# Kernel optimization log

Hardware: AMD Instinct MI355X
Metric: run time of the kernel (lower is better)

Reference implementation:

```python
import jax, jax.numpy as jnp
import numpy as np

NUM_EMB = 16384
EMB_DIM = 64
BETA = 0.25  # commitment_cost, legacy=True formulation


def _l2norm(x, axis=-1):
    # matches F.normalize(p=2): x / max(||x||, 1e-12)
    n = jnp.sqrt(jnp.sum(x * x, axis=axis, keepdims=True))
    return x / jnp.maximum(n, 1e-12)


def setup_inputs() -> dict:
    key = jax.random.key(0)
    k_z, k_cb, k_w, k_b = jax.random.split(key, 4)
    z = jax.random.normal(k_z, (16, 1024, EMB_DIM), dtype=jnp.float32)
    # frozen codebook: N(0, d^{-0.5})
    codebook = jax.random.normal(k_cb, (NUM_EMB, EMB_DIM), dtype=jnp.float32) * (EMB_DIM ** -0.5)
    # Linear(d, d) default init: U(-1/sqrt(d), 1/sqrt(d))
    lim = 1.0 / np.sqrt(EMB_DIM)
    proj_w = jax.random.uniform(k_w, (EMB_DIM, EMB_DIM), dtype=jnp.float32, minval=-lim, maxval=lim)
    proj_b = jax.random.uniform(k_b, (EMB_DIM,), dtype=jnp.float32, minval=-lim, maxval=lim)
    scale = jnp.float32(10.0)  # l2_norm_scale
    return {"z": z, "codebook": codebook, "proj_w": proj_w, "proj_b": proj_b, "scale": scale}


def reference(z, codebook, proj_w, proj_b, scale):
    B, T, d = z.shape
    zf = z.reshape(-1, d)                                   # [BT, d]
    quant_codebook = codebook @ proj_w.T + proj_b           # [N, d]
    zn = _l2norm(zf)
    cn = _l2norm(quant_codebook)
    distances = -jnp.einsum('bd,nd->bn', zn, cn) * scale    # [BT, N]
    idx = jnp.argmin(distances, axis=1)                     # [BT]
    quantized = quant_codebook[idx].reshape(z.shape)        # [B, T, d]
    sg = jax.lax.stop_gradient
    commitment_loss = jnp.mean((sg(quantized) - z) ** 2)
    codebook_loss = jnp.mean((quantized - sg(z)) ** 2)
    vq_loss = commitment_loss + BETA * codebook_loss        # legacy=True
    quantized_st = z + sg(quantized - z)                    # straight-through
    return quantized_st, vq_loss, idx.reshape(B, T)
```

## Files before the change

kernel.cpp:

```cpp
#include <hip/hip_runtime.h>
#include <hip/hip_bf16.h>


#define NCODES 16384
#define NTOK   16384
#define DIM    64
#define MARGIN_MFMA 8e-3f
#define CAP    16

typedef __attribute__((ext_vector_type(8))) short bf16x8;
typedef __attribute__((ext_vector_type(4))) float f32x4;
#define GLOBAL_AS __attribute__((address_space(1)))
#define LDS_AS    __attribute__((address_space(3)))

__device__ float  g_qcb[NCODES * DIM];
__device__ short  g_cnb[NCODES * DIM];
__device__ short  g_znb[NTOK * DIM];
__device__ unsigned g_topu[NTOK];
__device__ int    g_candcnt[NTOK];
__device__ int    g_cand[NTOK * CAP];
__device__ float  g_loss;
__device__ int    g_done;

__device__ __forceinline__ float wave_sum64(float v) {
#pragma unroll
  for (int o = 32; o > 0; o >>= 1) v += __shfl_xor(v, o, 64);
  return v;
}
__device__ __forceinline__ short f2bf(float f) {
  __hip_bfloat16 h = __float2bfloat16(f);
  return *reinterpret_cast<short*>(&h);
}
__device__ __forceinline__ float bf2f(short s) {
  __hip_bfloat16 h = *reinterpret_cast<__hip_bfloat16*>(&s);
  return __bfloat162float(h);
}
__device__ __forceinline__ void split8(const float* v, bf16x8& hi, bf16x8& lo) {
#pragma unroll
  for (int i = 0; i < 8; ++i) {
    float f = v[i];
    short h = f2bf(f);
    hi[i] = h;
    lo[i] = f2bf(f - bf2f(h));
  }
}

__global__ __launch_bounds__(256) void k_prep(const float* __restrict__ cb,
                                              const float* __restrict__ pw,
                                              const float* __restrict__ pb,
                                              const float* __restrict__ z) {
  int tid = threadIdx.x;
  int wave = tid >> 6, lane = tid & 63, quad = lane >> 4, col = lane & 15;
  if (blockIdx.x < 256) {
    int rowBase = blockIdx.x * 64 + wave * 16;
    const float* cr = cb + (size_t)(rowBase + col) * 64 + quad * 8;
    bf16x8 ah0, al0, ah1, al1;
    split8(cr, ah0, al0);
    split8(cr + 32, ah1, al1);
    float vals[4][4];
    float nr[4] = {0.f, 0.f, 0.f, 0.f};
    const f32x4 fz = {0.f, 0.f, 0.f, 0.f};
#pragma unroll
    for (int nt = 0; nt < 4; ++nt) {
      int j = col + 16 * nt;
      const float* wr = pw + (size_t)j * 64 + quad * 8;
      bf16x8 bh0, bl0, bh1, bl1;
      split8(wr, bh0, bl0);
      split8(wr + 32, bh1, bl1);
      f32x4 d = __builtin_amdgcn_mfma_f32_16x16x32_bf16(ah0, bh0, fz, 0, 0, 0);
      d = __builtin_amdgcn_mfma_f32_16x16x32_bf16(ah1, bh1, d, 0, 0, 0);
      d = __builtin_amdgcn_mfma_f32_16x16x32_bf16(ah0, bl0, d, 0, 0, 0);
      d = __builtin_amdgcn_mfma_f32_16x16x32_bf16(ah1, bl1, d, 0, 0, 0);
      d = __builtin_amdgcn_mfma_f32_16x16x32_bf16(al0, bh0, d, 0, 0, 0);
      d = __builtin_amdgcn_mfma_f32_16x16x32_bf16(al1, bh1, d, 0, 0, 0);
      float bj = pb[j];
#pragma unroll
      for (int r = 0; r < 4; ++r) {
        float v = d[r] + bj;
        vals[nt][r] = v;
        nr[r] = fmaf(v, v, nr[r]);
      }
    }
#pragma unroll
    for (int r = 0; r < 4; ++r) {
      float v = nr[r];
      v += __shfl_xor(v, 1, 64);
      v += __shfl_xor(v, 2, 64);
      v += __shfl_xor(v, 4, 64);
      v += __shfl_xor(v, 8, 64);
      nr[r] = 1.0f / fmaxf(sqrtf(v), 1e-12f);
    }
#pragma unroll
    for (int nt = 0; nt < 4; ++nt)
#pragma unroll
      for (int r = 0; r < 4; ++r) {
        int row = rowBase + quad * 4 + r;
        int j = col + 16 * nt;
        g_qcb[(size_t)row * 64 + j] = vals[nt][r];
        g_cnb[(size_t)row * 64 + j] = f2bf(vals[nt][r] * nr[r]);
      }
  } else {
    int zb = blockIdx.x - 256;
    int gid = zb * 256 + tid;
    if (gid < NTOK) { g_topu[gid] = 0u; g_candcnt[gid] = 0; }
    if (gid == 0) { g_loss = 0.f; g_done = 0; }
    int base = zb * 64;
    for (int r = 0; r < 16; ++r) {
      int row = base + wave * 16 + r;
      float v = z[(size_t)row * 64 + lane];
      float tot = wave_sum64(v * v);
      g_znb[(size_t)row * 64 + lane] = f2bf(v / fmaxf(sqrtf(tot), 1e-12f));
    }
  }
}

__global__ __launch_bounds__(256) void k_mfma1() {
  __shared__ __align__(16) short smB[2][8192];
  int tid = threadIdx.x;
  int wave = tid >> 6, lane = tid & 63;
  int quad = lane >> 4, col = lane & 15;
  int tokBlock = blockIdx.x >> 3, split = blockIdx.x & 7;
  int tokBase = tokBlock * 128 + wave * 32;

  const short* za = g_znb + (size_t)(tokBase + col) * 64 + quad * 8;
  bf16x8 A0[2], A1[2];
#pragma unroll
  for (int f = 0; f < 2; ++f) {
    A0[f] = *(const bf16x8*)(za + f * 16 * 64);
    A1[f] = *(const bf16x8*)(za + f * 16 * 64 + 32);
  }
  float m[2][4];
#pragma unroll
  for (int f = 0; f < 2; ++f)
#pragma unroll
    for (int r = 0; r < 4; ++r) m[f][r] = -3.0e38f;

  const char* gsplit = (const char*)(g_cnb + (size_t)split * 2048 * 64);
  int x = col & 7;
  int s0off = ((quad ^ x) << 3);
  int s1off = (((4 | quad) ^ x) << 3);
  int goff[4];
#pragma unroll
  for (int i = 0; i < 4; ++i) {
    int cidx = wave * 256 + i * 64 + lane;
    int row = cidx >> 3, sw = cidx & 7;
    goff[i] = row * 128 + ((sw ^ (row & 7)) << 4);
  }

#pragma unroll
  for (int i = 0; i < 4; ++i)
    __builtin_amdgcn_global_load_lds((const GLOBAL_AS void*)(gsplit + goff[i]),
                                     (LDS_AS void*)(&smB[0][wave * 2048 + i * 512]), 16, 0, 0);
  __syncthreads();

  int p = 0;
  for (int s = 0; s < 16; ++s) {
    if (s < 15) {
      const char* gb = gsplit + (size_t)(s + 1) * 16384;
#pragma unroll
      for (int i = 0; i < 4; ++i)
        __builtin_amdgcn_global_load_lds((const GLOBAL_AS void*)(gb + goff[i]),
                                         (LDS_AS void*)(&smB[p ^ 1][wave * 2048 + i * 512]),
                                         16, 0, 0);
    }
    const short* bufp = smB[p];
#pragma unroll
    for (int t = 0; t < 8; ++t) {
      const short* lb = bufp + (t * 16 + col) * 64;
      bf16x8 b0 = *(const bf16x8*)(lb + s0off);
      bf16x8 b1 = *(const bf16x8*)(lb + s1off);
#pragma unroll
      for (int f = 0; f < 2; ++f) {
        f32x4 acc = {0.f, 0.f, 0.f, 0.f};
        acc = __builtin_amdgcn_mfma_f32_16x16x32_bf16(A0[f], b0, acc, 0, 0, 0);
        acc = __builtin_amdgcn_mfma_f32_16x16x32_bf16(A1[f], b1, acc, 0, 0, 0);
#pragma unroll
        for (int r = 0; r < 4; ++r) m[f][r] = fmaxf(m[f][r], acc[r]);
      }
    }
    __syncthreads();
    p ^= 1;
  }

#pragma unroll
  for (int f = 0; f < 2; ++f)
#pragma unroll
    for (int r = 0; r < 4; ++r) {
      float v = m[f][r];
      v = fmaxf(v, __shfl_xor(v, 1, 64));
      v = fmaxf(v, __shfl_xor(v, 2, 64));
      v = fmaxf(v, __shfl_xor(v, 4, 64));
      v = fmaxf(v, __shfl_xor(v, 8, 64));
      if (col == 0) {
        unsigned b = __float_as_uint(v);
        unsigned e = (b & 0x80000000u) ? ~b : (b | 0x80000000u);
        atomicMax(&g_topu[tokBase + f * 16 + quad * 4 + r], e);
      }
    }
}

__global__ __launch_bounds__(256) void k_mfma2() {
  __shared__ __align__(16) short smB[2][8192];
  int tid = threadIdx.x;
  int wave = tid >> 6, lane = tid & 63;
  int quad = lane >> 4, col = lane & 15;
  int tokBlock = blockIdx.x >> 3, split = blockIdx.x & 7;
  int tokBase = tokBlock * 128 + wave * 32;

  const short* za = g_znb + (size_t)(tokBase + col) * 64 + quad * 8;
  bf16x8 A0[2], A1[2];
#pragma unroll
  for (int f = 0; f < 2; ++f) {
    A0[f] = *(const bf16x8*)(za + f * 16 * 64);
    A1[f] = *(const bf16x8*)(za + f * 16 * 64 + 32);
  }
  float th[2][4];
#pragma unroll
  for (int f = 0; f < 2; ++f)
#pragma unroll
    for (int r = 0; r < 4; ++r) {
      unsigned u = g_topu[tokBase + f * 16 + quad * 4 + r];
      unsigned b = (u & 0x80000000u) ? (u & 0x7FFFFFFFu) : ~u;
      th[f][r] = __uint_as_float(b) - MARGIN_MFMA;
    }

  const char* gsplit = (const char*)(g_cnb + (size_t)split * 2048 * 64);
  int x = col & 7;
  int s0off = ((quad ^ x) << 3);
  int s1off = (((4 | quad) ^ x) << 3);
  int goff[4];
#pragma unroll
  for (int i = 0; i < 4; ++i) {
    int cidx = wave * 256 + i * 64 + lane;
    int row = cidx >> 3, sw = cidx & 7;
    goff[i] = row * 128 + ((sw ^ (row & 7)) << 4);
  }

#pragma unroll
  for (int i = 0; i < 4; ++i)
    __builtin_amdgcn_global_load_lds((const GLOBAL_AS void*)(gsplit + goff[i]),
                                     (LDS_AS void*)(&smB[0][wave * 2048 + i * 512]), 16, 0, 0);
  __syncthreads();

  int codeB = split * 2048 + col;
  int p = 0;
  for (int s = 0; s < 16; ++s) {
    if (s < 15) {
      const char* gb = gsplit + (size_t)(s + 1) * 16384;
#pragma unroll
      for (int i = 0; i < 4; ++i)
        __builtin_amdgcn_global_load_lds((const GLOBAL_AS void*)(gb + goff[i]),
                                         (LDS_AS void*)(&smB[p ^ 1][wave * 2048 + i * 512]),
                                         16, 0, 0);
    }
    const short* bufp = smB[p];
#pragma unroll
    for (int t = 0; t < 8; ++t) {
      const short* lb = bufp + (t * 16 + col) * 64;
      bf16x8 b0 = *(const bf16x8*)(lb + s0off);
      bf16x8 b1 = *(const bf16x8*)(lb + s1off);
      int code = codeB + s * 128 + t * 16;
#pragma unroll
      for (int f = 0; f < 2; ++f) {
        f32x4 acc = {0.f, 0.f, 0.f, 0.f};
        acc = __builtin_amdgcn_mfma_f32_16x16x32_bf16(A0[f], b0, acc, 0, 0, 0);
        acc = __builtin_amdgcn_mfma_f32_16x16x32_bf16(A1[f], b1, acc, 0, 0, 0);
        float dmax = fmaxf(fmaxf(acc[0] - th[f][0], acc[1] - th[f][1]),
                           fmaxf(acc[2] - th[f][2], acc[3] - th[f][3]));
        if (dmax >= 0.f) {
#pragma unroll
          for (int r = 0; r < 4; ++r) {
            if (acc[r] >= th[f][r]) {
              int tok = tokBase + f * 16 + quad * 4 + r;
              int pos = atomicAdd(&g_candcnt[tok], 1);
              if (pos < CAP) g_cand[tok * CAP + pos] = code;
            }
          }
        }
      }
    }
    __syncthreads();
    p ^= 1;
  }
}

__global__ __launch_bounds__(256) void k_final(const float* __restrict__ z,
                                               const float* __restrict__ cb,
                                               const float* __restrict__ pw,
                                               const float* __restrict__ pb,
                                               float* __restrict__ out0,
                                               float* __restrict__ out1,
                                               float* __restrict__ out2) {
  __shared__ double Wl[64 * 65];
  __shared__ float cbl[4][64];
  int tid = threadIdx.x;
  int wave = tid >> 6, lane = tid & 63;

  for (int e = tid; e < 4096; e += 256) {
    int j = e >> 6, k = e & 63;
    Wl[j * 65 + k] = (double)pw[(size_t)j * 64 + k];
  }
  __syncthreads();

  double bj = (double)pb[lane];
  int wg = blockIdx.x * 4 + wave;
  float lsum = 0.f;

  for (int i = 0; i < 4; ++i) {
    int tok = wg * 4 + i;
    int cnt = g_candcnt[tok];
    int idx;
    if (cnt <= 1) {
      idx = g_cand[tok * CAP];
    } else {
      double zj = (double)z[(size_t)tok * 64 + lane];
      double best = -1.0e300;
      int bi = 0x7FFFFFFF;
      int lim = (cnt <= CAP) ? cnt : 0;
      for (int c = 0; c < lim; ++c) {
        int code = g_cand[tok * CAP + c];
        cbl[wave][lane] = cb[(size_t)code * 64 + lane];
        double qc = bj;
#pragma unroll 16
        for (int k = 0; k < 64; ++k)
          qc = fma(Wl[lane * 65 + k], (double)cbl[wave][k], qc);
        double s = zj * qc, n2 = qc * qc;
#pragma unroll
        for (int o = 32; o > 0; o >>= 1) {
          s += __shfl_xor(s, o, 64);
          n2 += __shfl_xor(n2, o, 64);
        }
        double key = s / fmax(sqrt(n2), 1e-12);
        if (key > best || (key == best && code < bi)) { best = key; bi = code; }
      }
      if (cnt > CAP) {
        for (int code = 0; code < NCODES; ++code) {
          cbl[wave][lane] = cb[(size_t)code * 64 + lane];
          double qc = bj;
#pragma unroll 16
          for (int k = 0; k < 64; ++k)
            qc = fma(Wl[lane * 65 + k], (double)cbl[wave][k], qc);
          double s = zj * qc, n2 = qc * qc;
#pragma unroll
          for (int o = 32; o > 0; o >>= 1) {
            s += __shfl_xor(s, o, 64);
            n2 += __shfl_xor(n2, o, 64);
          }
          double key = s / fmax(sqrt(n2), 1e-12);
          if (key > best || (key == best && code < bi)) { best = key; bi = code; }
        }
      }
      idx = bi;
    }
    float q = g_qcb[(size_t)idx * 64 + lane];
    float zv = z[(size_t)tok * 64 + lane];
    float d = q - zv;
    out0[(size_t)tok * 64 + lane] = zv + d;
    lsum = fmaf(d, d, lsum);
    if (lane == 0) out2[tok] = (float)idx;
  }
  float tot = wave_sum64(lsum);
  if (lane == 0) atomicAdd(&g_loss, tot);
  __syncthreads();
  if (tid == 0) {
    __threadfence();
    int d = atomicAdd(&g_done, 1);
    if (d == (int)gridDim.x - 1) {
      __threadfence();
      float lv = atomicAdd(&g_loss, 0.0f);
      out1[0] = 1.25f * lv / 1048576.0f;
    }
  }
}

extern "C" void kernel_launch(void* const* d_in, const int* in_sizes, int n_in,
                              void* d_out, int out_size, void* d_ws, size_t ws_size,
                              hipStream_t stream) {
  const float* z = (const float*)d_in[0];
  const float* cb = (const float*)d_in[1];
  const float* pw = (const float*)d_in[2];
  const float* pb = (const float*)d_in[3];

  float* out0 = (float*)d_out;
  float* out1 = out0 + (size_t)NTOK * DIM;
  float* out2 = out1 + 1;

  hipLaunchKernelGGL(k_prep, dim3(512), dim3(256), 0, stream, cb, pw, pb, z);
  hipLaunchKernelGGL(k_mfma1, dim3(1024), dim3(256), 0, stream);
  hipLaunchKernelGGL(k_mfma2, dim3(1024), dim3(256), 0, stream);
  hipLaunchKernelGGL(k_final, dim3(1024), dim3(256), 0, stream, z, cb, pw, pb, out0, out1, out2);
}
```

Measured before the change: 232.0 us.

## Compact ambiguous tokens into a worklist and split final stage into kernels

The final stage is split in four. A scan kernel builds a compacted worklist of tokens that have two or more candidates. An arbitration kernel then spreads only those tokens across all waves, using a transposed fp64 weight tile and four independent FMA chains to cut the dependency latency. Output writing and the loss reduction become separate kernels, using per-block partials instead of global atomics and a done-counter. This is meant to remove the load imbalance where a few waves did the slow fp64 re-ranking, at the cost of three extra kernel launches.

```diff
diff --git a/kernel.cpp b/kernel.cpp
--- a/kernel.cpp
+++ b/kernel.cpp
@@ -19,8 +19,9 @@
 __device__ unsigned g_topu[NTOK];
 __device__ int    g_candcnt[NTOK];
 __device__ int    g_cand[NTOK * CAP];
-__device__ float  g_loss;
-__device__ int    g_done;
+__device__ int    g_wl[NTOK];
+__device__ int    g_wln;
+__device__ float  g_partial[512];
 
 __device__ __forceinline__ float wave_sum64(float v) {
 #pragma unroll
@@ -103,7 +104,7 @@
     int zb = blockIdx.x - 256;
     int gid = zb * 256 + tid;
     if (gid < NTOK) { g_topu[gid] = 0u; g_candcnt[gid] = 0; }
-    if (gid == 0) { g_loss = 0.f; g_done = 0; }
+    if (gid == 0) g_wln = 0;
     int base = zb * 64;
     for (int r = 0; r < 16; ++r) {
       int row = base + wave * 16 + r;
@@ -284,46 +285,85 @@
   }
 }
 
-__global__ __launch_bounds__(256) void k_final(const float* __restrict__ z,
-                                               const float* __restrict__ cb,
-                                               const float* __restrict__ pw,
-                                               const float* __restrict__ pb,
-                                               float* __restrict__ out0,
-                                               float* __restrict__ out1,
-                                               float* __restrict__ out2) {
-  __shared__ double Wl[64 * 65];
+__global__ __launch_bounds__(256) void k_scan() {
+  __shared__ int flags[256];
+  __shared__ int sbase;
+  int tid = threadIdx.x;
+  int tok = blockIdx.x * 256 + tid;
+  int flag = (g_candcnt[tok] >= 2) ? 1 : 0;
+  flags[tid] = flag;
+  __syncthreads();
+  if (tid == 0) {
+    int run = 0;
+    for (int i = 0; i < 256; ++i) {
+      int f = flags[i];
+      flags[i] = run;
+      run += f;
+    }
+    sbase = atomicAdd(&g_wln, run);
+  }
+  __syncthreads();
+  if (flag) g_wl[sbase + flags[tid]] = tok;
+}
+
+__global__ __launch_bounds__(256) void k_arb(const float* __restrict__ z,
+                                             const float* __restrict__ cb,
+                                             const float* __restrict__ pw,
+                                             const float* __restrict__ pb) {
+  __shared__ double WT[64 * 65];
   __shared__ float cbl[4][64];
   int tid = threadIdx.x;
   int wave = tid >> 6, lane = tid & 63;
-
   for (int e = tid; e < 4096; e += 256) {
     int j = e >> 6, k = e & 63;
-    Wl[j * 65 + k] = (double)pw[(size_t)j * 64 + k];
-  }
-  __syncthreads();
-
+    WT[k * 65 + j] = (double)pw[e];
+  }
+  __syncthreads();
+
+  int wln = g_wln;
   double bj = (double)pb[lane];
-  int wg = blockIdx.x * 4 + wave;
-  float lsum = 0.f;
-
-  for (int i = 0; i < 4; ++i) {
-    int tok = wg * 4 + i;
+  int gwave = blockIdx.x * 4 + wave;
+
+  for (int e = gwave; e < wln; e += 1024) {
+    int tok = g_wl[e];
     int cnt = g_candcnt[tok];
-    int idx;
-    if (cnt <= 1) {
-      idx = g_cand[tok * CAP];
-    } else {
-      double zj = (double)z[(size_t)tok * 64 + lane];
-      double best = -1.0e300;
-      int bi = 0x7FFFFFFF;
-      int lim = (cnt <= CAP) ? cnt : 0;
-      for (int c = 0; c < lim; ++c) {
-        int code = g_cand[tok * CAP + c];
+    double zj = (double)z[(size_t)tok * 64 + lane];
+    double best = -1.0e300;
+    int bi = 0x7FFFFFFF;
+    int lim = (cnt <= CAP) ? cnt : 0;
+    for (int c = 0; c < lim; ++c) {
+      int code = g_cand[tok * CAP + c];
+      cbl[wave][lane] = cb[(size_t)code * 64 + lane];
+      double s0 = 0.0, s1 = 0.0, s2 = 0.0, s3 = 0.0;
+#pragma unroll
+      for (int kk = 0; kk < 16; ++kk) {
+        s0 = fma(WT[kk * 65 + lane], (double)cbl[wave][kk], s0);
+        s1 = fma(WT[(kk + 16) * 65 + lane], (double)cbl[wave][kk + 16], s1);
+        s2 = fma(WT[(kk + 32) * 65 + lane], (double)cbl[wave][kk + 32], s2);
+        s3 = fma(WT[(kk + 48) * 65 + lane], (double)cbl[wave][kk + 48], s3);
+      }
+      double qc = ((s0 + s1) + (s2 + s3)) + bj;
+      double s = zj * qc, n2 = qc * qc;
+#pragma unroll
+      for (int o = 32; o > 0; o >>= 1) {
+        s += __shfl_xor(s, o, 64);
+        n2 += __shfl_xor(n2, o, 64);
+      }
+      double key = s / fmax(sqrt(n2), 1e-12);
+      if (key > best || (key == best && code < bi)) { best = key; bi = code; }
+    }
+    if (cnt > CAP) {
+      for (int code = 0; code < NCODES; ++code) {
         cbl[wave][lane] = cb[(size_t)code * 64 + lane];
-        double qc = bj;
-#pragma unroll 16
-        for (int k = 0; k < 64; ++k)
-          qc = fma(Wl[lane * 65 + k], (double)cbl[wave][k], qc);
+        double s0 = 0.0, s1 = 0.0, s2 = 0.0, s3 = 0.0;
+#pragma unroll
+        for (int kk = 0; kk < 16; ++kk) {
+          s0 = fma(WT[kk * 65 + lane], (double)cbl[wave][kk], s0);
+          s1 = fma(WT[(kk + 16) * 65 + lane], (double)cbl[wave][kk + 16], s1);
+          s2 = fma(WT[(kk + 32) * 65 + lane], (double)cbl[wave][kk + 32], s2);
+          s3 = fma(WT[(kk + 48) * 65 + lane], (double)cbl[wave][kk + 48], s3);
+        }
+        double qc = ((s0 + s1) + (s2 + s3)) + bj;
         double s = zj * qc, n2 = qc * qc;
 #pragma unroll
         for (int o = 32; o > 0; o >>= 1) {
@@ -333,25 +373,22 @@
         double key = s / fmax(sqrt(n2), 1e-12);
         if (key > best || (key == best && code < bi)) { best = key; bi = code; }
       }
-      if (cnt > CAP) {
-        for (int code = 0; code < NCODES; ++code) {
-          cbl[wave][lane] = cb[(size_t)code * 64 + lane];
-          double qc = bj;
-#pragma unroll 16
-          for (int k = 0; k < 64; ++k)
-            qc = fma(Wl[lane * 65 + k], (double)cbl[wave][k], qc);
-          double s = zj * qc, n2 = qc * qc;
-#pragma unroll
-          for (int o = 32; o > 0; o >>= 1) {
-            s += __shfl_xor(s, o, 64);
-            n2 += __shfl_xor(n2, o, 64);
-          }
-          double key = s / fmax(sqrt(n2), 1e-12);
-          if (key > best || (key == best && code < bi)) { best = key; bi = code; }
-        }
-      }
-      idx = bi;
-    }
+    }
+    if (lane == 0) g_cand[tok * CAP] = bi;
+  }
+}
+
+__global__ __launch_bounds__(256) void k_out(const float* __restrict__ z,
+                                             float* __restrict__ out0,
+                                             float* __restrict__ out2) {
+  __shared__ float ws[4];
+  int tid = threadIdx.x;
+  int wave = tid >> 6, lane = tid & 63;
+  int base = blockIdx.x * 32;
+  float lsum = 0.f;
+  for (int r = 0; r < 8; ++r) {
+    int tok = base + wave * 8 + r;
+    int idx = g_cand[tok * CAP];
     float q = g_qcb[(size_t)idx * 64 + lane];
     float zv = z[(size_t)tok * 64 + lane];
     float d = q - zv;
@@ -360,17 +397,18 @@
     if (lane == 0) out2[tok] = (float)idx;
   }
   float tot = wave_sum64(lsum);
-  if (lane == 0) atomicAdd(&g_loss, tot);
-  __syncthreads();
-  if (tid == 0) {
-    __threadfence();
-    int d = atomicAdd(&g_done, 1);
-    if (d == (int)gridDim.x - 1) {
-      __threadfence();
-      float lv = atomicAdd(&g_loss, 0.0f);
-      out1[0] = 1.25f * lv / 1048576.0f;
-    }
-  }
+  if (lane == 0) ws[wave] = tot;
+  __syncthreads();
+  if (tid == 0) g_partial[blockIdx.x] = ((ws[0] + ws[1]) + (ws[2] + ws[3]));
+}
+
+__global__ void k_loss(float* __restrict__ out1) {
+  int lane = threadIdx.x;
+  float s = 0.f;
+#pragma unroll
+  for (int i = 0; i < 8; ++i) s += g_partial[lane + 64 * i];
+  s = wave_sum64(s);
+  if (lane == 0) out1[0] = 1.25f * s / 1048576.0f;
 }
 
 extern "C" void kernel_launch(void* const* d_in, const int* in_sizes, int n_in,
@@ -388,5 +426,8 @@
   hipLaunchKernelGGL(k_prep, dim3(512), dim3(256), 0, stream, cb, pw, pb, z);
   hipLaunchKernelGGL(k_mfma1, dim3(1024), dim3(256), 0, stream);
   hipLaunchKernelGGL(k_mfma2, dim3(1024), dim3(256), 0, stream);
-  hipLaunchKernelGGL(k_final, dim3(1024), dim3(256), 0, stream, z, cb, pw, pb, out0, out1, out2);
-}
+  hipLaunchKernelGGL(k_scan, dim3(64), dim3(256), 0, stream);
+  hipLaunchKernelGGL(k_arb, dim3(256), dim3(256), 0, stream, z, cb, pw, pb);
+  hipLaunchKernelGGL(k_out, dim3(512), dim3(256), 0, stream, z, out0, out2);
+  hipLaunchKernelGGL(k_loss, dim3(1), dim3(64), 0, stream, out1);
+}
```

New measurement: 203.3 us. 1.14x faster.
